# Performance work log

Measured on AMD Instinct MI355X. Metric: run time of the kernel, lower is better.

The kernel has to match this reference:

```python
import jax, jax.numpy as jnp
import numpy as np

NEG_SLOPE = 0.2  # PyG GATConv default LeakyReLU negative slope
NUM_GRAPHS = 256


def gat_conv(x, edge_src, edge_dst, W, att_src, att_dst, bias):
    """PyG-style GATConv. x:[N,Fin], W:[H*C,Fin], att_*:[H,C], bias:[H*C]."""
    N = x.shape[0]
    H, C = att_src.shape
    h = (x @ W.T).reshape(N, H, C)                       # [N,H,C]
    a_src = jnp.sum(h * att_src, axis=-1)                # [N,H]
    a_dst = jnp.sum(h * att_dst, axis=-1)                # [N,H]
    e = jax.nn.leaky_relu(a_src[edge_src] + a_dst[edge_dst], NEG_SLOPE)  # [E,H]
    # segment softmax over edges sharing the same destination node
    m = jax.ops.segment_max(e, edge_dst, num_segments=N)
    ex = jnp.exp(e - m[edge_dst])
    den = jax.ops.segment_sum(ex, edge_dst, num_segments=N)
    alpha = ex / (den[edge_dst] + 1e-16)                 # [E,H]
    out = jax.ops.segment_sum(h[edge_src] * alpha[..., None], edge_dst,
                              num_segments=N)            # [N,H,C]
    return out.reshape(N, H * C) + bias


def setup_inputs() -> dict:
    key = jax.random.key(0)
    ks = jax.random.split(key, 16)
    N, E, Fin = 20000, 320000, 128
    H1, C1 = 8, 64          # conv1: heads=8, hidden_dim1=64 -> concat 512
    D1 = H1 * C1            # 512
    D2 = 128                # hidden_dim2, conv2 heads=1
    OUT = 2
    s = lambda k, shp, fan: jax.random.normal(k, shp, jnp.float32) * (1.0 / np.sqrt(fan))
    x = jax.random.normal(ks[0], (N, Fin), jnp.float32)
    edge_index = jax.random.randint(ks[1], (2, E), 0, N, jnp.int32)
    batch = jnp.sort(jax.random.randint(ks[2], (N,), 0, NUM_GRAPHS, jnp.int32))
    return {
        "x": x, "edge_index": edge_index, "batch": batch,
        "W1": s(ks[3], (D1, Fin), Fin), "att_src1": s(ks[4], (H1, C1), C1),
        "att_dst1": s(ks[5], (H1, C1), C1), "b1": jnp.zeros((D1,), jnp.float32),
        "W2": s(ks[6], (D2, D1), D1), "att_src2": s(ks[7], (1, D2), D2),
        "att_dst2": s(ks[8], (1, D2), D2), "b2": jnp.zeros((D2,), jnp.float32),
        "w_attn": s(ks[9], (D2, 1), D2), "b_attn": jnp.zeros((1,), jnp.float32),
        "w_mask": s(ks[10], (D2, 1), D2), "b_mask": jnp.zeros((1,), jnp.float32),
        "W_out": s(ks[11], (OUT, D2), D2), "b_out": jnp.zeros((OUT,), jnp.float32),
    }


def reference(x, edge_index, batch, W1, att_src1, att_dst1, b1,
              W2, att_src2, att_dst2, b2, w_attn, b_attn, w_mask, b_mask,
              W_out, b_out):
    N = x.shape[0]
    loops = jnp.arange(N, dtype=edge_index.dtype)
    src = jnp.concatenate([edge_index[0], loops])  # PyG add_self_loops=True
    dst = jnp.concatenate([edge_index[1], loops])

    h = gat_conv(x, src, dst, W1, att_src1, att_dst1, b1)   # [N, 512]
    h = jax.nn.relu(h)                                      # dropout = identity (eval)
    h = gat_conv(h, src, dst, W2, att_src2, att_dst2, b2)   # [N, 128]
    h = jax.nn.relu(h)

    # attention pooling over graphs in the batch
    attn_scores = h @ w_attn + b_attn                       # [N,1]
    node_mask = jax.nn.sigmoid(h @ w_mask + b_mask)         # [N,1]
    weighted = h * (attn_scores * node_mask)                # [N,128]
    pooled = jax.ops.segment_sum(weighted, batch, num_segments=NUM_GRAPHS)
    return pooled @ W_out.T + b_out                         # [256, 2]
```

## Files before the change

kernel.cpp:

```cpp
#include <hip/hip_runtime.h>
#include <math.h>


#define NEG_SLOPE 0.2f
#define LDSB 40

using bf16x8 = __attribute__((ext_vector_type(8))) __bf16;
using f32x4  = __attribute__((ext_vector_type(4))) float;

__device__ __forceinline__ ushort f2bf(float f) {
    unsigned u = __float_as_uint(f);
    unsigned r = (u + 0x7FFFu + ((u >> 16) & 1u)) >> 16;
    return (ushort)r;
}
__device__ __forceinline__ unsigned pack2(float a, float b) {
    return (unsigned)f2bf(a) | ((unsigned)f2bf(b) << 16);
}
__device__ __forceinline__ float bflo(unsigned u) { return __uint_as_float(u << 16); }
__device__ __forceinline__ float bfhi(unsigned u) { return __uint_as_float(u & 0xFFFF0000u); }
__device__ __forceinline__ void unpack8(uint4 u, float* f) {
    f[0] = bflo(u.x); f[1] = bfhi(u.x);
    f[2] = bflo(u.y); f[3] = bfhi(u.y);
    f[4] = bflo(u.z); f[5] = bfhi(u.z);
    f[6] = bflo(u.w); f[7] = bfhi(u.w);
}
__device__ __forceinline__ void unpack4(uint2 u, float* f) {
    f[0] = bflo(u.x); f[1] = bfhi(u.x);
    f[2] = bflo(u.y); f[3] = bfhi(u.y);
}

__global__ __launch_bounds__(256) void prep(const float* __restrict__ x, ushort* __restrict__ xb, int nx4,
                                            const float* __restrict__ w1, ushort* __restrict__ w1b, int nw14,
                                            const float* __restrict__ w2, ushort* __restrict__ w2b, int nw24,
                                            int cvtBlocks,
                                            const int* __restrict__ edst, int* __restrict__ cnt, int E) {
    int blk = blockIdx.x;
    if (blk < cvtBlocks) {
        int j = blk * 256 + threadIdx.x;
        const float* src; ushort* dst;
        if (j < nx4) { src = x; dst = xb; }
        else {
            j -= nx4;
            if (j < nw14) { src = w1; dst = w1b; }
            else {
                j -= nw14;
                if (j >= nw24) return;
                src = w2; dst = w2b;
            }
        }
        float4 v = ((const float4*)src)[j];
        uint2 o;
        o.x = pack2(v.x, v.y);
        o.y = pack2(v.z, v.w);
        ((uint2*)dst)[j] = o;
    } else {
        int e = (blk - cvtBlocks) * 256 + threadIdx.x;
        if (e < E) atomicAdd(&cnt[edst[e]], 1);
    }
}

__device__ __forceinline__ void gemm_body(ushort* As, ushort* Bs,
                                          const ushort* __restrict__ A,
                                          const ushort* __restrict__ B,
                                          ushort* __restrict__ C,
                                          int M, int N, int K, int bx, int by,
                                          const float* __restrict__ att_s,
                                          const float* __restrict__ att_d,
                                          float* __restrict__ sout,
                                          float* __restrict__ dout, int H) {
    int t = threadIdx.x;
    int wave = t >> 6, lane = t & 63;
    int quad = lane >> 4, l16 = lane & 15;
    int m0 = bx * 128, n0 = by * 128;
    int wm = (wave & 1) * 64;
    int wn = (wave >> 1) * 64;
    int srow = t >> 1;
    int sseg = (t & 1) * 16;
    int growA = m0 + srow;
    bool okA = growA < M;
    f32x4 acc[4][4] = {};
    uint4 av0, av1, bv0, bv1;
    {
        if (okA) {
            const uint4* gp = (const uint4*)(A + (size_t)growA * K + sseg);
            av0 = gp[0]; av1 = gp[1];
        } else { av0 = make_uint4(0, 0, 0, 0); av1 = av0; }
        const uint4* gq = (const uint4*)(B + (size_t)(n0 + srow) * K + sseg);
        bv0 = gq[0]; bv1 = gq[1];
    }
    for (int k0 = 0; k0 < K; k0 += 32) {
        __syncthreads();
        *(uint4*)&As[srow * LDSB + sseg]     = av0;
        *(uint4*)&As[srow * LDSB + sseg + 8] = av1;
        *(uint4*)&Bs[srow * LDSB + sseg]     = bv0;
        *(uint4*)&Bs[srow * LDSB + sseg + 8] = bv1;
        __syncthreads();
        int k1 = k0 + 32;
        if (k1 < K) {
            if (okA) {
                const uint4* gp = (const uint4*)(A + (size_t)growA * K + k1 + sseg);
                av0 = gp[0]; av1 = gp[1];
            } else { av0 = make_uint4(0, 0, 0, 0); av1 = av0; }
            const uint4* gq = (const uint4*)(B + (size_t)(n0 + srow) * K + k1 + sseg);
            bv0 = gq[0]; bv1 = gq[1];
        }
        bf16x8 af[4], bf[4];
#pragma unroll
        for (int i = 0; i < 4; ++i)
            af[i] = *(const bf16x8*)&As[(wm + i * 16 + l16) * LDSB + quad * 8];
#pragma unroll
        for (int j = 0; j < 4; ++j)
            bf[j] = *(const bf16x8*)&Bs[(wn + j * 16 + l16) * LDSB + quad * 8];
#pragma unroll
        for (int i = 0; i < 4; ++i)
#pragma unroll
            for (int j = 0; j < 4; ++j)
                acc[i][j] = __builtin_amdgcn_mfma_f32_16x16x32_bf16(
                    af[i], bf[j], acc[i][j], 0, 0, 0);
    }
#pragma unroll
    for (int i = 0; i < 4; ++i) {
#pragma unroll
        for (int r = 0; r < 4; ++r) {
            int grow = m0 + wm + i * 16 + quad * 4 + r;
            if (grow < M) {
#pragma unroll
                for (int j = 0; j < 4; ++j) {
                    int gcol = n0 + wn + j * 16 + l16;
                    C[(size_t)grow * N + gcol] = f2bf(acc[i][j][r]);
                }
            }
        }
    }
    float as[4], adw[4];
#pragma unroll
    for (int j = 0; j < 4; ++j) {
        int col = n0 + wn + j * 16 + l16;
        as[j]  = att_s[col];
        adw[j] = att_d[col];
    }
    int head = (H == 8) ? ((n0 + wn) >> 6) : 0;
#pragma unroll
    for (int i = 0; i < 4; ++i) {
#pragma unroll
        for (int r = 0; r < 4; ++r) {
            float ps = acc[i][0][r] * as[0] + acc[i][1][r] * as[1] +
                       acc[i][2][r] * as[2] + acc[i][3][r] * as[3];
            float pd = acc[i][0][r] * adw[0] + acc[i][1][r] * adw[1] +
                       acc[i][2][r] * adw[2] + acc[i][3][r] * adw[3];
#pragma unroll
            for (int off = 1; off < 16; off <<= 1) {
                ps += __shfl_xor(ps, off);
                pd += __shfl_xor(pd, off);
            }
            int grow = m0 + wm + i * 16 + quad * 4 + r;
            if (l16 == 0 && grow < M) {
                if (H == 1) {
                    atomicAdd(&sout[grow], ps);
                    atomicAdd(&dout[grow], pd);
                } else {
                    sout[grow * 8 + head] = ps;
                    dout[grow * 8 + head] = pd;
                }
            }
        }
    }
}

__global__ __launch_bounds__(256) void g1f(const ushort* __restrict__ A,
                                           const ushort* __restrict__ B,
                                           ushort* __restrict__ C,
                                           int M, int N, int K,
                                           const float* __restrict__ att_s,
                                           const float* __restrict__ att_d,
                                           float* __restrict__ sout,
                                           float* __restrict__ dout, int H,
                                           int gemmBlocks, int nby,
                                           const int* __restrict__ esrc,
                                           const int* __restrict__ edst,
                                           int* __restrict__ cursor,
                                           int* __restrict__ srcs, int E) {
    __shared__ ushort As[128 * LDSB];
    __shared__ ushort Bs[128 * LDSB];
    int blk = blockIdx.x;
    if (blk < gemmBlocks) {
        gemm_body(As, Bs, A, B, C, M, N, K, blk / nby, blk % nby,
                  att_s, att_d, sout, dout, H);
    } else {
        int e = (blk - gemmBlocks) * 256 + threadIdx.x;
        if (e < E) {
            int pos = atomicAdd(&cursor[edst[e]], 1);
            srcs[pos] = esrc[e];
        }
    }
}

__global__ __launch_bounds__(256) void gemm_k(const ushort* __restrict__ A,
                                              const ushort* __restrict__ B,
                                              ushort* __restrict__ C,
                                              int M, int N, int K,
                                              const float* __restrict__ att_s,
                                              const float* __restrict__ att_d,
                                              float* __restrict__ sout,
                                              float* __restrict__ dout, int H,
                                              int nby) {
    __shared__ ushort As[128 * LDSB];
    __shared__ ushort Bs[128 * LDSB];
    gemm_body(As, Bs, A, B, C, M, N, K, blockIdx.x / nby, blockIdx.x % nby,
              att_s, att_d, sout, dout, H);
}

__global__ __launch_bounds__(1024) void scan_offsets(const int* cnt, int* row_start,
                                                     int* cursor, int N) {
    __shared__ int sm[1024];
    int t = threadIdx.x;
    int per = (N + 1023) / 1024;
    int beg = t * per;
    int end = beg + per; if (end > N) end = N;
    int sum = 0;
    for (int i = beg; i < end; ++i) sum += cnt[i];
    sm[t] = sum;
    __syncthreads();
    for (int off = 1; off < 1024; off <<= 1) {
        int add = (t >= off) ? sm[t - off] : 0;
        __syncthreads();
        sm[t] += add;
        __syncthreads();
    }
    int run = sm[t] - sum;
    for (int i = beg; i < end; ++i) {
        int c = cnt[i];
        row_start[i] = run;
        cursor[i] = run;
        run += c;
    }
    if (t == 1023) row_start[N] = run;
}

__global__ __launch_bounds__(256) void agg1(const ushort* __restrict__ h1,
                                            const float* __restrict__ a1s,
                                            const float* __restrict__ a1d,
                                            const int* __restrict__ row_start,
                                            const int* __restrict__ srcs,
                                            const float* __restrict__ b1,
                                            ushort* __restrict__ r1, int N) {
    int node = blockIdx.x * 4 + (threadIdx.x >> 6);
    if (node >= N) return;
    int lane = threadIdx.x & 63;
    int head = lane >> 3;
    int f0 = lane * 8;
    int pbeg = row_start[node], pend = row_start[node + 1];
    float ad = a1d[node * 8 + head];
    float es = a1s[node * 8 + head] + ad;
    es = es > 0.f ? es : NEG_SLOPE * es;
    float ex_self = __expf(es);
    float den = ex_self;
    float q[8];
    unpack8(*(const uint4*)(h1 + (size_t)node * 512 + f0), q);
    float acc[8];
#pragma unroll
    for (int j = 0; j < 8; ++j) acc[j] = ex_self * q[j];
    int p = pbeg;
    for (; p + 4 <= pend; p += 4) {
        int s0 = srcs[p + 0];
        int s1 = srcs[p + 1];
        int s2 = srcs[p + 2];
        int s3 = srcs[p + 3];
        uint4 u0 = *(const uint4*)(h1 + (size_t)s0 * 512 + f0);
        uint4 u1 = *(const uint4*)(h1 + (size_t)s1 * 512 + f0);
        uint4 u2 = *(const uint4*)(h1 + (size_t)s2 * 512 + f0);
        uint4 u3 = *(const uint4*)(h1 + (size_t)s3 * 512 + f0);
        float as0 = a1s[s0 * 8 + head];
        float as1 = a1s[s1 * 8 + head];
        float as2 = a1s[s2 * 8 + head];
        float as3 = a1s[s3 * 8 + head];
        float e0 = as0 + ad; e0 = e0 > 0.f ? e0 : NEG_SLOPE * e0;
        float e1 = as1 + ad; e1 = e1 > 0.f ? e1 : NEG_SLOPE * e1;
        float e2 = as2 + ad; e2 = e2 > 0.f ? e2 : NEG_SLOPE * e2;
        float e3 = as3 + ad; e3 = e3 > 0.f ? e3 : NEG_SLOPE * e3;
        float x0 = __expf(e0), x1 = __expf(e1), x2 = __expf(e2), x3 = __expf(e3);
        den += (x0 + x1) + (x2 + x3);
        float v[8];
        unpack8(u0, v);
#pragma unroll
        for (int j = 0; j < 8; ++j) acc[j] += x0 * v[j];
        unpack8(u1, v);
#pragma unroll
        for (int j = 0; j < 8; ++j) acc[j] += x1 * v[j];
        unpack8(u2, v);
#pragma unroll
        for (int j = 0; j < 8; ++j) acc[j] += x2 * v[j];
        unpack8(u3, v);
#pragma unroll
        for (int j = 0; j < 8; ++j) acc[j] += x3 * v[j];
    }
    for (; p < pend; ++p) {
        int s = srcs[p];
        float e = a1s[s * 8 + head] + ad;
        e = e > 0.f ? e : NEG_SLOPE * e;
        float ex = __expf(e);
        den += ex;
        float v[8];
        unpack8(*(const uint4*)(h1 + (size_t)s * 512 + f0), v);
#pragma unroll
        for (int j = 0; j < 8; ++j) acc[j] += ex * v[j];
    }
    float rden = 1.0f / (den + 1e-16f);
    const float4* bp = (const float4*)(b1 + f0);
    float4 b0 = bp[0], b1v = bp[1];
    float o[8];
    o[0] = fmaxf(acc[0] * rden + b0.x, 0.f);
    o[1] = fmaxf(acc[1] * rden + b0.y, 0.f);
    o[2] = fmaxf(acc[2] * rden + b0.z, 0.f);
    o[3] = fmaxf(acc[3] * rden + b0.w, 0.f);
    o[4] = fmaxf(acc[4] * rden + b1v.x, 0.f);
    o[5] = fmaxf(acc[5] * rden + b1v.y, 0.f);
    o[6] = fmaxf(acc[6] * rden + b1v.z, 0.f);
    o[7] = fmaxf(acc[7] * rden + b1v.w, 0.f);
    uint4 ov;
    ov.x = pack2(o[0], o[1]); ov.y = pack2(o[2], o[3]);
    ov.z = pack2(o[4], o[5]); ov.w = pack2(o[6], o[7]);
    *(uint4*)(r1 + (size_t)node * 512 + f0) = ov;
}

__global__ __launch_bounds__(256) void agg2pool(const ushort* __restrict__ h2,
                                                const float* __restrict__ a2s,
                                                const float* __restrict__ a2d,
                                                const int* __restrict__ row_start,
                                                const int* __restrict__ srcs,
                                                const float* __restrict__ b2,
                                                const int* __restrict__ batch,
                                                const float* __restrict__ w_attn,
                                                const float* __restrict__ b_attn,
                                                const float* __restrict__ w_mask,
                                                const float* __restrict__ b_mask,
                                                float* __restrict__ pooled, int N) {
    int node = blockIdx.x * 8 + (threadIdx.x >> 5);
    if (node >= N) return;
    int sub = threadIdx.x & 31;
    int f0 = sub * 4;
    int pbeg = row_start[node], pend = row_start[node + 1];
    float ad = a2d[node];
    float es = a2s[node] + ad;
    es = es > 0.f ? es : NEG_SLOPE * es;
    float ex_self = __expf(es);
    float den = ex_self;
    float q[4];
    unpack4(*(const uint2*)(h2 + (size_t)node * 128 + f0), q);
    float acc[4];
#pragma unroll
    for (int j = 0; j < 4; ++j) acc[j] = ex_self * q[j];
    int p = pbeg;
    for (; p + 4 <= pend; p += 4) {
        int s0 = srcs[p + 0];
        int s1 = srcs[p + 1];
        int s2 = srcs[p + 2];
        int s3 = srcs[p + 3];
        uint2 u0 = *(const uint2*)(h2 + (size_t)s0 * 128 + f0);
        uint2 u1 = *(const uint2*)(h2 + (size_t)s1 * 128 + f0);
        uint2 u2 = *(const uint2*)(h2 + (size_t)s2 * 128 + f0);
        uint2 u3 = *(const uint2*)(h2 + (size_t)s3 * 128 + f0);
        float as0 = a2s[s0];
        float as1 = a2s[s1];
        float as2 = a2s[s2];
        float as3 = a2s[s3];
        float e0 = as0 + ad; e0 = e0 > 0.f ? e0 : NEG_SLOPE * e0;
        float e1 = as1 + ad; e1 = e1 > 0.f ? e1 : NEG_SLOPE * e1;
        float e2 = as2 + ad; e2 = e2 > 0.f ? e2 : NEG_SLOPE * e2;
        float e3 = as3 + ad; e3 = e3 > 0.f ? e3 : NEG_SLOPE * e3;
        float x0 = __expf(e0), x1 = __expf(e1), x2 = __expf(e2), x3 = __expf(e3);
        den += (x0 + x1) + (x2 + x3);
        float v[4];
        unpack4(u0, v);
#pragma unroll
        for (int j = 0; j < 4; ++j) acc[j] += x0 * v[j];
        unpack4(u1, v);
#pragma unroll
        for (int j = 0; j < 4; ++j) acc[j] += x1 * v[j];
        unpack4(u2, v);
#pragma unroll
        for (int j = 0; j < 4; ++j) acc[j] += x2 * v[j];
        unpack4(u3, v);
#pragma unroll
        for (int j = 0; j < 4; ++j) acc[j] += x3 * v[j];
    }
    for (; p < pend; ++p) {
        int s = srcs[p];
        float e = a2s[s] + ad;
        e = e > 0.f ? e : NEG_SLOPE * e;
        float ex = __expf(e);
        den += ex;
        float v[4];
        unpack4(*(const uint2*)(h2 + (size_t)s * 128 + f0), v);
#pragma unroll
        for (int j = 0; j < 4; ++j) acc[j] += ex * v[j];
    }
    float rden = 1.0f / (den + 1e-16f);
    float4 bv = *(const float4*)(b2 + f0);
    float4 o;
    o.x = fmaxf(acc[0] * rden + bv.x, 0.f);
    o.y = fmaxf(acc[1] * rden + bv.y, 0.f);
    o.z = fmaxf(acc[2] * rden + bv.z, 0.f);
    o.w = fmaxf(acc[3] * rden + bv.w, 0.f);
    float4 wa = *(const float4*)(w_attn + f0);
    float4 wm = *(const float4*)(w_mask + f0);
    float pa = o.x * wa.x + o.y * wa.y + o.z * wa.z + o.w * wa.w;
    float pm = o.x * wm.x + o.y * wm.y + o.z * wm.z + o.w * wm.w;
#pragma unroll
    for (int off = 1; off < 32; off <<= 1) {
        pa += __shfl_xor(pa, off);
        pm += __shfl_xor(pm, off);
    }
    float attn = pa + b_attn[0];
    float mask = 1.0f / (1.0f + __expf(-(pm + b_mask[0])));
    float w = attn * mask;
    int g = batch[node];
    float* pg = pooled + (size_t)g * 128 + f0;
    atomicAdd(pg + 0, o.x * w);
    atomicAdd(pg + 1, o.y * w);
    atomicAdd(pg + 2, o.z * w);
    atomicAdd(pg + 3, o.w * w);
}

__global__ void final_kernel(const float* __restrict__ pooled,
                             const float* __restrict__ W_out,
                             const float* __restrict__ b_out,
                             float* __restrict__ out) {
    int tid = blockIdx.x * 256 + threadIdx.x;
    if (tid >= 512) return;
    int g = tid >> 1, o = tid & 1;
    const float* p = pooled + g * 128;
    const float* w = W_out + o * 128;
    float s = 0.f;
#pragma unroll 4
    for (int f = 0; f < 128; ++f) s += p[f] * w[f];
    out[tid] = s + b_out[o];
}

extern "C" void kernel_launch(void* const* d_in, const int* in_sizes, int n_in,
                              void* d_out, int out_size, void* d_ws, size_t ws_size,
                              hipStream_t stream) {
    const float* x        = (const float*)d_in[0];
    const int* edge_index = (const int*)d_in[1];
    const int* batch      = (const int*)d_in[2];
    const float* W1       = (const float*)d_in[3];
    const float* att_src1 = (const float*)d_in[4];
    const float* att_dst1 = (const float*)d_in[5];
    const float* b1       = (const float*)d_in[6];
    const float* W2       = (const float*)d_in[7];
    const float* att_src2 = (const float*)d_in[8];
    const float* att_dst2 = (const float*)d_in[9];
    const float* b2       = (const float*)d_in[10];
    const float* w_attn   = (const float*)d_in[11];
    const float* b_attn   = (const float*)d_in[12];
    const float* w_mask   = (const float*)d_in[13];
    const float* b_mask   = (const float*)d_in[14];
    const float* W_out    = (const float*)d_in[15];
    const float* b_out    = (const float*)d_in[16];
    float* out = (float*)d_out;

    int N = in_sizes[0] / 128;
    int E = in_sizes[1] / 2;
    const int* esrc = edge_index;
    const int* edst = edge_index + E;

    char* ws = (char*)d_ws;
    size_t off = 0;
    auto alloc = [&](size_t bytes) {
        void* p = ws + off;
        off = (off + bytes + 255) & ~(size_t)255;
        return p;
    };
    ushort* h1       = (ushort*)alloc((size_t)N * 512 * 2);
    ushort* r1       = (ushort*)alloc((size_t)N * 512 * 2);
    ushort* h2       = (ushort*)alloc((size_t)N * 128 * 2);
    ushort* xb       = (ushort*)alloc((size_t)N * 128 * 2);
    ushort* w1b      = (ushort*)alloc((size_t)512 * 128 * 2);
    ushort* w2b      = (ushort*)alloc((size_t)128 * 512 * 2);
    float*  a1s      = (float*)alloc((size_t)N * 8 * 4);
    float*  a1d      = (float*)alloc((size_t)N * 8 * 4);
    int*    row_start= (int*)alloc((size_t)(N + 1) * 4);
    int*    srcs     = (int*)alloc((size_t)E * 4);
    int*    cursor   = (int*)alloc((size_t)N * 4);
    float*  a2s      = (float*)alloc((size_t)N * 4);
    float*  a2d      = (float*)alloc((size_t)N * 4);
    float*  pooled   = (float*)alloc((size_t)256 * 128 * 4);
    size_t zspan = (size_t)((char*)(pooled + 256 * 128) - (char*)cursor);
    hipMemsetAsync(cursor, 0, zspan, stream);

    dim3 b256(256);
    int nx4 = N * 128 / 4;
    int nw4 = 512 * 128 / 4;
    int cvtBlocks = (nx4 + 2 * nw4 + 255) / 256;
    int cntBlocks = (E + 255) / 256;
    prep<<<cvtBlocks + cntBlocks, b256, 0, stream>>>(x, xb, nx4, W1, w1b, nw4,
                                                     W2, w2b, nw4, cvtBlocks,
                                                     edst, cursor, E);
    scan_offsets<<<1, 1024, 0, stream>>>(cursor, row_start, cursor, N);
    int g1Blocks = ((N + 127) / 128) * 4;
    g1f<<<g1Blocks + cntBlocks, b256, 0, stream>>>(xb, w1b, h1, N, 512, 128,
                                                   att_src1, att_dst1, a1s, a1d, 8,
                                                   g1Blocks, 4,
                                                   esrc, edst, cursor, srcs, E);
    agg1<<<(N + 3) / 4, b256, 0, stream>>>(h1, a1s, a1d, row_start, srcs, b1, r1, N);
    gemm_k<<<(N + 127) / 128, b256, 0, stream>>>(r1, w2b, h2, N, 128, 512,
                                                 att_src2, att_dst2, a2s, a2d, 1, 1);
    agg2pool<<<(N + 7) / 8, b256, 0, stream>>>(h2, a2s, a2d, row_start, srcs, b2,
                                               batch, w_attn, b_attn, w_mask, b_mask,
                                               pooled, N);
    final_kernel<<<2, b256, 0, stream>>>(pooled, W_out, b_out, out);
}
```

Baseline: 291.1 us.

## Fold output projection into layer-2 aggregation and batch neighbor loads by eight

Uses linearity to apply the final W_out projection per node inside the layer-2 aggregation kernel, atomically adding two scalars per node into the output instead of 128 floats per node into a pooled buffer. This removes the final kernel, the pooled buffer and its memset, and output initialisation with b_out moves into the scan kernel. The neighbor loop is also rewritten to issue eight predicated gathers at a time for more memory-level parallelism, at the cost of wasted loads on tail iterations. Contention on 512 output addresses rises, and float atomic ordering changes the rounding.

```diff
diff --git a/kernel.cpp b/kernel.cpp
--- a/kernel.cpp
+++ b/kernel.cpp
@@ -211,9 +211,12 @@
 }
 
 __global__ __launch_bounds__(1024) void scan_offsets(const int* cnt, int* row_start,
-                                                     int* cursor, int N) {
+                                                     int* cursor, int N,
+                                                     const float* __restrict__ b_out,
+                                                     float* __restrict__ out) {
     __shared__ int sm[1024];
     int t = threadIdx.x;
+    if (t < 512) out[t] = b_out[t & 1];
     int per = (N + 1023) / 1024;
     int beg = t * per;
     int end = beg + per; if (end > N) end = N;
@@ -323,18 +326,19 @@
     *(uint4*)(r1 + (size_t)node * 512 + f0) = ov;
 }
 
-__global__ __launch_bounds__(256) void agg2pool(const ushort* __restrict__ h2,
-                                                const float* __restrict__ a2s,
-                                                const float* __restrict__ a2d,
-                                                const int* __restrict__ row_start,
-                                                const int* __restrict__ srcs,
-                                                const float* __restrict__ b2,
-                                                const int* __restrict__ batch,
-                                                const float* __restrict__ w_attn,
-                                                const float* __restrict__ b_attn,
-                                                const float* __restrict__ w_mask,
-                                                const float* __restrict__ b_mask,
-                                                float* __restrict__ pooled, int N) {
+__global__ __launch_bounds__(256) void agg2out(const ushort* __restrict__ h2,
+                                               const float* __restrict__ a2s,
+                                               const float* __restrict__ a2d,
+                                               const int* __restrict__ row_start,
+                                               const int* __restrict__ srcs,
+                                               const float* __restrict__ b2,
+                                               const int* __restrict__ batch,
+                                               const float* __restrict__ w_attn,
+                                               const float* __restrict__ b_attn,
+                                               const float* __restrict__ w_mask,
+                                               const float* __restrict__ b_mask,
+                                               const float* __restrict__ W_out,
+                                               float* __restrict__ out, int N) {
     int node = blockIdx.x * 8 + (threadIdx.x >> 5);
     if (node >= N) return;
     int sub = threadIdx.x & 31;
@@ -350,50 +354,32 @@
     float acc[4];
 #pragma unroll
     for (int j = 0; j < 4; ++j) acc[j] = ex_self * q[j];
-    int p = pbeg;
-    for (; p + 4 <= pend; p += 4) {
-        int s0 = srcs[p + 0];
-        int s1 = srcs[p + 1];
-        int s2 = srcs[p + 2];
-        int s3 = srcs[p + 3];
-        uint2 u0 = *(const uint2*)(h2 + (size_t)s0 * 128 + f0);
-        uint2 u1 = *(const uint2*)(h2 + (size_t)s1 * 128 + f0);
-        uint2 u2 = *(const uint2*)(h2 + (size_t)s2 * 128 + f0);
-        uint2 u3 = *(const uint2*)(h2 + (size_t)s3 * 128 + f0);
-        float as0 = a2s[s0];
-        float as1 = a2s[s1];
-        float as2 = a2s[s2];
-        float as3 = a2s[s3];
-        float e0 = as0 + ad; e0 = e0 > 0.f ? e0 : NEG_SLOPE * e0;
-        float e1 = as1 + ad; e1 = e1 > 0.f ? e1 : NEG_SLOPE * e1;
-        float e2 = as2 + ad; e2 = e2 > 0.f ? e2 : NEG_SLOPE * e2;
-        float e3 = as3 + ad; e3 = e3 > 0.f ? e3 : NEG_SLOPE * e3;
-        float x0 = __expf(e0), x1 = __expf(e1), x2 = __expf(e2), x3 = __expf(e3);
-        den += (x0 + x1) + (x2 + x3);
-        float v[4];
-        unpack4(u0, v);
-#pragma unroll
-        for (int j = 0; j < 4; ++j) acc[j] += x0 * v[j];
-        unpack4(u1, v);
-#pragma unroll
-        for (int j = 0; j < 4; ++j) acc[j] += x1 * v[j];
-        unpack4(u2, v);
-#pragma unroll
-        for (int j = 0; j < 4; ++j) acc[j] += x2 * v[j];
-        unpack4(u3, v);
-#pragma unroll
-        for (int j = 0; j < 4; ++j) acc[j] += x3 * v[j];
-    }
-    for (; p < pend; ++p) {
-        int s = srcs[p];
-        float e = a2s[s] + ad;
-        e = e > 0.f ? e : NEG_SLOPE * e;
-        float ex = __expf(e);
-        den += ex;
-        float v[4];
-        unpack4(*(const uint2*)(h2 + (size_t)s * 128 + f0), v);
-#pragma unroll
-        for (int j = 0; j < 4; ++j) acc[j] += ex * v[j];
+    for (int p = pbeg; p < pend; p += 8) {
+        int sidx[8]; bool okb[8];
+#pragma unroll
+        for (int k = 0; k < 8; ++k) {
+            int pk = p + k;
+            okb[k] = pk < pend;
+            sidx[k] = srcs[okb[k] ? pk : pbeg];
+        }
+        uint2 u[8];
+#pragma unroll
+        for (int k = 0; k < 8; ++k)
+            u[k] = *(const uint2*)(h2 + (size_t)sidx[k] * 128 + f0);
+        float sc[8];
+#pragma unroll
+        for (int k = 0; k < 8; ++k) sc[k] = a2s[sidx[k]];
+#pragma unroll
+        for (int k = 0; k < 8; ++k) {
+            float e = sc[k] + ad;
+            e = e > 0.f ? e : NEG_SLOPE * e;
+            float xk = okb[k] ? __expf(e) : 0.f;
+            den += xk;
+            float v[4];
+            unpack4(u[k], v);
+#pragma unroll
+            for (int j = 0; j < 4; ++j) acc[j] += xk * v[j];
+        }
     }
     float rden = 1.0f / (den + 1e-16f);
     float4 bv = *(const float4*)(b2 + f0);
@@ -404,37 +390,27 @@
     o.w = fmaxf(acc[3] * rden + bv.w, 0.f);
     float4 wa = *(const float4*)(w_attn + f0);
     float4 wm = *(const float4*)(w_mask + f0);
+    float4 w0 = *(const float4*)(W_out + f0);
+    float4 w1 = *(const float4*)(W_out + 128 + f0);
     float pa = o.x * wa.x + o.y * wa.y + o.z * wa.z + o.w * wa.w;
     float pm = o.x * wm.x + o.y * wm.y + o.z * wm.z + o.w * wm.w;
+    float d0 = o.x * w0.x + o.y * w0.y + o.z * w0.z + o.w * w0.w;
+    float d1 = o.x * w1.x + o.y * w1.y + o.z * w1.z + o.w * w1.w;
 #pragma unroll
     for (int off = 1; off < 32; off <<= 1) {
         pa += __shfl_xor(pa, off);
         pm += __shfl_xor(pm, off);
-    }
-    float attn = pa + b_attn[0];
-    float mask = 1.0f / (1.0f + __expf(-(pm + b_mask[0])));
-    float w = attn * mask;
-    int g = batch[node];
-    float* pg = pooled + (size_t)g * 128 + f0;
-    atomicAdd(pg + 0, o.x * w);
-    atomicAdd(pg + 1, o.y * w);
-    atomicAdd(pg + 2, o.z * w);
-    atomicAdd(pg + 3, o.w * w);
-}
-
-__global__ void final_kernel(const float* __restrict__ pooled,
-                             const float* __restrict__ W_out,
-                             const float* __restrict__ b_out,
-                             float* __restrict__ out) {
-    int tid = blockIdx.x * 256 + threadIdx.x;
-    if (tid >= 512) return;
-    int g = tid >> 1, o = tid & 1;
-    const float* p = pooled + g * 128;
-    const float* w = W_out + o * 128;
-    float s = 0.f;
-#pragma unroll 4
-    for (int f = 0; f < 128; ++f) s += p[f] * w[f];
-    out[tid] = s + b_out[o];
+        d0 += __shfl_xor(d0, off);
+        d1 += __shfl_xor(d1, off);
+    }
+    if (sub == 0) {
+        float attn = pa + b_attn[0];
+        float mask = 1.0f / (1.0f + __expf(-(pm + b_mask[0])));
+        float w = attn * mask;
+        int g = batch[node];
+        atomicAdd(&out[g * 2 + 0], w * d0);
+        atomicAdd(&out[g * 2 + 1], w * d1);
+    }
 }
 
 extern "C" void kernel_launch(void* const* d_in, const int* in_sizes, int n_in,
@@ -484,8 +460,7 @@
     int*    cursor   = (int*)alloc((size_t)N * 4);
     float*  a2s      = (float*)alloc((size_t)N * 4);
     float*  a2d      = (float*)alloc((size_t)N * 4);
-    float*  pooled   = (float*)alloc((size_t)256 * 128 * 4);
-    size_t zspan = (size_t)((char*)(pooled + 256 * 128) - (char*)cursor);
+    size_t zspan = (size_t)((char*)(a2d + N) - (char*)cursor);
     hipMemsetAsync(cursor, 0, zspan, stream);
 
     dim3 b256(256);
@@ -496,7 +471,7 @@
     prep<<<cvtBlocks + cntBlocks, b256, 0, stream>>>(x, xb, nx4, W1, w1b, nw4,
                                                      W2, w2b, nw4, cvtBlocks,
                                                      edst, cursor, E);
-    scan_offsets<<<1, 1024, 0, stream>>>(cursor, row_start, cursor, N);
+    scan_offsets<<<1, 1024, 0, stream>>>(cursor, row_start, cursor, N, b_out, out);
     int g1Blocks = ((N + 127) / 128) * 4;
     g1f<<<g1Blocks + cntBlocks, b256, 0, stream>>>(xb, w1b, h1, N, 512, 128,
                                                    att_src1, att_dst1, a1s, a1d, 8,
@@ -505,8 +480,7 @@
     agg1<<<(N + 3) / 4, b256, 0, stream>>>(h1, a1s, a1d, row_start, srcs, b1, r1, N);
     gemm_k<<<(N + 127) / 128, b256, 0, stream>>>(r1, w2b, h2, N, 128, 512,
                                                  att_src2, att_dst2, a2s, a2d, 1, 1);
-    agg2pool<<<(N + 7) / 8, b256, 0, stream>>>(h2, a2s, a2d, row_start, srcs, b2,
-                                               batch, w_attn, b_attn, w_mask, b_mask,
-                                               pooled, N);
-    final_kernel<<<2, b256, 0, stream>>>(pooled, W_out, b_out, out);
-}
+    agg2out<<<(N + 7) / 8, b256, 0, stream>>>(h2, a2s, a2d, row_start, srcs, b2,
+                                              batch, w_attn, b_attn, w_mask, b_mask,
+                                              W_out, out, N);
+}
```

New measurement: 290.9 us. Within noise of the previous version (-0.1%).

## Fold output projection into aggregation kernel, drop pooled buffer and final kernel

Applied to the files above, without the earlier changes.

Because the output layer is linear, each node's weighted features are projected through W_out inside the second aggregation kernel. Only two atomic adds per node go straight into the output, replacing 128 per-feature atomics into a pooled buffer. The separate final kernel and the pooled memset are removed, and the bias is written into the output early from the scan kernel. Floating-point summation order changes, and the correctness of the bias initialisation relies on the scan kernel running before the aggregation kernel on the same stream.

```diff
diff --git a/kernel.cpp b/kernel.cpp
--- a/kernel.cpp
+++ b/kernel.cpp
@@ -211,9 +211,12 @@
 }
 
 __global__ __launch_bounds__(1024) void scan_offsets(const int* cnt, int* row_start,
-                                                     int* cursor, int N) {
+                                                     int* cursor, int N,
+                                                     const float* __restrict__ b_out,
+                                                     float* __restrict__ out) {
     __shared__ int sm[1024];
     int t = threadIdx.x;
+    if (t < 512) out[t] = b_out[t & 1];
     int per = (N + 1023) / 1024;
     int beg = t * per;
     int end = beg + per; if (end > N) end = N;
@@ -323,18 +326,19 @@
     *(uint4*)(r1 + (size_t)node * 512 + f0) = ov;
 }
 
-__global__ __launch_bounds__(256) void agg2pool(const ushort* __restrict__ h2,
-                                                const float* __restrict__ a2s,
-                                                const float* __restrict__ a2d,
-                                                const int* __restrict__ row_start,
-                                                const int* __restrict__ srcs,
-                                                const float* __restrict__ b2,
-                                                const int* __restrict__ batch,
-                                                const float* __restrict__ w_attn,
-                                                const float* __restrict__ b_attn,
-                                                const float* __restrict__ w_mask,
-                                                const float* __restrict__ b_mask,
-                                                float* __restrict__ pooled, int N) {
+__global__ __launch_bounds__(256) void agg2out(const ushort* __restrict__ h2,
+                                               const float* __restrict__ a2s,
+                                               const float* __restrict__ a2d,
+                                               const int* __restrict__ row_start,
+                                               const int* __restrict__ srcs,
+                                               const float* __restrict__ b2,
+                                               const int* __restrict__ batch,
+                                               const float* __restrict__ w_attn,
+                                               const float* __restrict__ b_attn,
+                                               const float* __restrict__ w_mask,
+                                               const float* __restrict__ b_mask,
+                                               const float* __restrict__ W_out,
+                                               float* __restrict__ out, int N) {
     int node = blockIdx.x * 8 + (threadIdx.x >> 5);
     if (node >= N) return;
     int sub = threadIdx.x & 31;
@@ -404,37 +408,27 @@
     o.w = fmaxf(acc[3] * rden + bv.w, 0.f);
     float4 wa = *(const float4*)(w_attn + f0);
     float4 wm = *(const float4*)(w_mask + f0);
+    float4 w0 = *(const float4*)(W_out + f0);
+    float4 w1 = *(const float4*)(W_out + 128 + f0);
     float pa = o.x * wa.x + o.y * wa.y + o.z * wa.z + o.w * wa.w;
     float pm = o.x * wm.x + o.y * wm.y + o.z * wm.z + o.w * wm.w;
+    float d0 = o.x * w0.x + o.y * w0.y + o.z * w0.z + o.w * w0.w;
+    float d1 = o.x * w1.x + o.y * w1.y + o.z * w1.z + o.w * w1.w;
 #pragma unroll
     for (int off = 1; off < 32; off <<= 1) {
         pa += __shfl_xor(pa, off);
         pm += __shfl_xor(pm, off);
-    }
-    float attn = pa + b_attn[0];
-    float mask = 1.0f / (1.0f + __expf(-(pm + b_mask[0])));
-    float w = attn * mask;
-    int g = batch[node];
-    float* pg = pooled + (size_t)g * 128 + f0;
-    atomicAdd(pg + 0, o.x * w);
-    atomicAdd(pg + 1, o.y * w);
-    atomicAdd(pg + 2, o.z * w);
-    atomicAdd(pg + 3, o.w * w);
-}
-
-__global__ void final_kernel(const float* __restrict__ pooled,
-                             const float* __restrict__ W_out,
-                             const float* __restrict__ b_out,
-                             float* __restrict__ out) {
-    int tid = blockIdx.x * 256 + threadIdx.x;
-    if (tid >= 512) return;
-    int g = tid >> 1, o = tid & 1;
-    const float* p = pooled + g * 128;
-    const float* w = W_out + o * 128;
-    float s = 0.f;
-#pragma unroll 4
-    for (int f = 0; f < 128; ++f) s += p[f] * w[f];
-    out[tid] = s + b_out[o];
+        d0 += __shfl_xor(d0, off);
+        d1 += __shfl_xor(d1, off);
+    }
+    if (sub == 0) {
+        float attn = pa + b_attn[0];
+        float mask = 1.0f / (1.0f + __expf(-(pm + b_mask[0])));
+        float w = attn * mask;
+        int g = batch[node];
+        atomicAdd(&out[g * 2 + 0], w * d0);
+        atomicAdd(&out[g * 2 + 1], w * d1);
+    }
 }
 
 extern "C" void kernel_launch(void* const* d_in, const int* in_sizes, int n_in,
@@ -484,8 +478,7 @@
     int*    cursor   = (int*)alloc((size_t)N * 4);
     float*  a2s      = (float*)alloc((size_t)N * 4);
     float*  a2d      = (float*)alloc((size_t)N * 4);
-    float*  pooled   = (float*)alloc((size_t)256 * 128 * 4);
-    size_t zspan = (size_t)((char*)(pooled + 256 * 128) - (char*)cursor);
+    size_t zspan = (size_t)((char*)(a2d + N) - (char*)cursor);
     hipMemsetAsync(cursor, 0, zspan, stream);
 
     dim3 b256(256);
@@ -496,7 +489,7 @@
     prep<<<cvtBlocks + cntBlocks, b256, 0, stream>>>(x, xb, nx4, W1, w1b, nw4,
                                                      W2, w2b, nw4, cvtBlocks,
                                                      edst, cursor, E);
-    scan_offsets<<<1, 1024, 0, stream>>>(cursor, row_start, cursor, N);
+    scan_offsets<<<1, 1024, 0, stream>>>(cursor, row_start, cursor, N, b_out, out);
     int g1Blocks = ((N + 127) / 128) * 4;
     g1f<<<g1Blocks + cntBlocks, b256, 0, stream>>>(xb, w1b, h1, N, 512, 128,
                                                    att_src1, att_dst1, a1s, a1d, 8,
@@ -505,8 +498,7 @@
     agg1<<<(N + 3) / 4, b256, 0, stream>>>(h1, a1s, a1d, row_start, srcs, b1, r1, N);
     gemm_k<<<(N + 127) / 128, b256, 0, stream>>>(r1, w2b, h2, N, 128, 512,
                                                  att_src2, att_dst2, a2s, a2d, 1, 1);
-    agg2pool<<<(N + 7) / 8, b256, 0, stream>>>(h2, a2s, a2d, row_start, srcs, b2,
-                                               batch, w_attn, b_attn, w_mask, b_mask,
-                                               pooled, N);
-    final_kernel<<<2, b256, 0, stream>>>(pooled, W_out, b_out, out);
-}
+    agg2out<<<(N + 7) / 8, b256, 0, stream>>>(h2, a2s, a2d, row_start, srcs, b2,
+                                              batch, w_attn, b_attn, w_mask, b_mask,
+                                              W_out, out, N);
+}
```

New measurement: 291.7 us. Within noise of the previous version (+0.2%).
